# Kernel optimization log

Measured on AMD Instinct MI355X. Metric: run time of the kernel, lower is better.

Reference implementation:

```python
import jax, jax.numpy as jnp
import numpy as np

B, L, D, H = 2, 2048, 1024, 16
HD = D // H


def setup_inputs() -> dict:
    key = jax.random.key(0)
    ks = jax.random.split(key, 12)
    s = 1.0 / np.sqrt(D)
    inp = {
        "q": jax.random.normal(ks[0], (B, L, D), jnp.float32),
        "k": jax.random.normal(ks[1], (B, L, D), jnp.float32),
        "v": jax.random.normal(ks[2], (B, L, D), jnp.float32),
        "mask": jnp.zeros((B, L), dtype=bool),  # True = masked out
        "Wq": jax.random.normal(ks[3], (D, D), jnp.float32) * s,
        "bq": jnp.zeros((D,), jnp.float32),
        "Wk": jax.random.normal(ks[4], (D, D), jnp.float32) * s,
        "bk": jnp.zeros((D,), jnp.float32),
        "Wv": jax.random.normal(ks[5], (D, D), jnp.float32) * s,
        "bv": jnp.zeros((D,), jnp.float32),
        "Wo": jax.random.normal(ks[6], (D, D), jnp.float32) * s,
        "bo": jnp.zeros((D,), jnp.float32),
    }
    return inp


def reference(q, k, v, mask, Wq, bq, Wk, bk, Wv, bv, Wo, bo):
    # linear projections (torch Linear: x @ W.T + b), split into heads: [B,H,L,HD]
    def proj(x, W, b):
        y = jnp.einsum('bld,ed->ble', x, W) + b
        return y.reshape(x.shape[0], x.shape[1], H, HD).transpose(0, 2, 1, 3)

    Q = proj(q, Wq, bq)
    K = proj(k, Wk, bk)
    V = proj(v, Wv, bv)

    scale = 1.0 / np.sqrt(HD).astype(np.float32)
    scores = jnp.einsum('bhqd,bhkd->bhqk', Q, K) * scale  # [B,H,Lq,Lk]
    # mask [B,Lk] -> broadcast over heads and query positions
    scores = jnp.where(mask[:, None, None, :], -jnp.inf, scores)
    attn = jax.nn.softmax(scores, axis=-1)
    out = jnp.einsum('bhqk,bhkd->bhqd', attn, V)  # [B,H,Lq,HD]
    out = out.transpose(0, 2, 1, 3).reshape(q.shape[0], q.shape[1], D)
    return jnp.einsum('bld,ed->ble', out, Wo) + bo
```

## Files before the change

### kernel.cpp

```cpp
#include <hip/hip_runtime.h>

#define LSEQ 2048
#define DMODEL 1024
#define NHEAD 16
#define HDIM 64

typedef __attribute__((ext_vector_type(8))) short bf16x8;
typedef __attribute__((ext_vector_type(4))) float f32x4;
typedef __attribute__((ext_vector_type(16))) float f32x16;
typedef unsigned int u32;
typedef unsigned short u16;
typedef unsigned long long u64;

static __device__ __forceinline__ u16 f2bf(float x) {
    return (u16)((__builtin_bit_cast(u32, x) + 0x8000u) >> 16);
}

static __device__ __forceinline__ u32 f2bf_pk(float hi, float lo) {
    u32 a = __builtin_bit_cast(u32, hi) + 0x8000u;
    u32 b = __builtin_bit_cast(u32, lo) + 0x8000u;
#if __has_builtin(__builtin_amdgcn_perm)
    return __builtin_amdgcn_perm(a, b, 0x07060302u);
#else
    return (a & 0xFFFF0000u) | (b >> 16);
#endif
}

static __device__ __forceinline__ float fast_exp2(float x) {
#if __has_builtin(__builtin_amdgcn_exp2f)
    return __builtin_amdgcn_exp2f(x);
#else
    return __expf(x * 0.6931471805599453f);
#endif
}

static __device__ __forceinline__ void gll16(const void* g, void* l) {
    __builtin_amdgcn_global_load_lds(
        (const __attribute__((address_space(1))) u32*)g,
        (__attribute__((address_space(3))) u32*)l, 16, 0, 0);
}

template <int N>
static __device__ __forceinline__ void vwait() {
    asm volatile("s_waitcnt vmcnt(%0)" :: "n"(N) : "memory");
}

__global__ __launch_bounds__(256) void conv_all(
    const float* __restrict__ q, const float* __restrict__ k, const float* __restrict__ v,
    const float* __restrict__ w0, const float* __restrict__ w1,
    const float* __restrict__ w2, const float* __restrict__ w3,
    u16* __restrict__ Qf, u16* __restrict__ Kf, u16* __restrict__ Vf,
    u16* __restrict__ o0, u16* __restrict__ o1, u16* __restrict__ o2,
    u16* __restrict__ o3) {
    const int bid = blockIdx.x;
    const float* s; u16* d; int off;
    if (bid < 12288) {
        const int z = bid >> 12;
        off = bid & 4095;
        if (z == 0)      { s = q; d = Qf; }
        else if (z == 1) { s = k; d = Kf; }
        else             { s = v; d = Vf; }
    } else {
        const int t = bid - 12288;
        const int z = t >> 10;
        off = t & 1023;
        if (z == 0)      { s = w0; d = o0; }
        else if (z == 1) { s = w1; d = o1; }
        else if (z == 2) { s = w2; d = o2; }
        else             { s = w3; d = o3; }
    }
    const int i = (off * 256 + threadIdx.x) * 4;
    float4 x = *(const float4*)(s + i);
    uint2 r;
    r.x = f2bf_pk(x.y, x.x);
    r.y = f2bf_pk(x.w, x.z);
    *(uint2*)(d + i) = r;
}

template <int OUT_MODE, int BN>
__device__ __forceinline__ void mfma_gemm(u16* __restrict__ sm,
                                          const u16* __restrict__ Xb,
                                          const u16* __restrict__ Wb,
                                          const float* __restrict__ bias,
                                          void* __restrict__ Yv, float scale) {
    constexpr int NB = BN / 32;
    constexpr int LPT = (BN == 128) ? 4 : 3;
    constexpr int ASZ = 4096;
    constexpr int BSZ = BN * 32;
    constexpr int NT = DMODEL / 32;
    u16* As = sm;
    u16* Bs = sm + 3 * ASZ;

    const int tid = threadIdx.x;
    const int wave = tid >> 6, lane = tid & 63;
    const int l16 = lane & 15, quad = lane >> 4;
    const int wm = (wave >> 1) * 64, wn = (wave & 1) * (BN / 2);
    const int m0 = blockIdx.x * 128, n0 = blockIdx.y * BN;

    const u16* Xr = Xb + (size_t)(m0 + (tid >> 2)) * DMODEL + (tid & 3) * 8;
    const u16* Wr = Wb + (size_t)(n0 + (tid >> 2)) * DMODEL + (tid & 3) * 8;
    const int t8 = tid * 8;

    auto stage = [&](int kt, int slot) {
        const int k0 = kt * 32;
        u16* Ab = As + slot * ASZ;
        u16* Bb = Bs + slot * BSZ;
        gll16(Xr + k0, Ab + t8);
        gll16(Xr + (size_t)64 * DMODEL + k0, Ab + 2048 + t8);
        gll16(Wr + k0, Bb + t8);
        if (BN == 128)
            gll16(Wr + (size_t)64 * DMODEL + k0, Bb + 2048 + t8);
    };

    f32x4 acc[4][NB];
    #pragma unroll
    for (int i = 0; i < 4; ++i)
        #pragma unroll
        for (int j = 0; j < NB; ++j)
            #pragma unroll
            for (int r = 0; r < 4; ++r) acc[i][j][r] = 0.0f;

    auto compute = [&](int kt) {
        const u16* Ac = As + (kt % 3) * ASZ;
        const u16* Bc = Bs + (kt % 3) * BSZ;
        bf16x8 af[4], bf[NB];
        #pragma unroll
        for (int mb = 0; mb < 4; ++mb)
            af[mb] = *(const bf16x8*)(Ac + (wm + mb * 16 + l16) * 32 + quad * 8);
        #pragma unroll
        for (int nb = 0; nb < NB; ++nb)
            bf[nb] = *(const bf16x8*)(Bc + (wn + nb * 16 + l16) * 32 + quad * 8);
        #pragma unroll
        for (int mb = 0; mb < 4; ++mb)
            #pragma unroll
            for (int nb = 0; nb < NB; ++nb)
                acc[mb][nb] = __builtin_amdgcn_mfma_f32_16x16x32_bf16(
                    af[mb], bf[nb], acc[mb][nb], 0, 0, 0);
    };

    stage(0, 0);
    stage(1, 1);

    #pragma unroll 1
    for (int kt = 0; kt < NT - 1; ++kt) {
        vwait<LPT>();
        __builtin_amdgcn_s_barrier();
        if (kt + 2 < NT) stage(kt + 2, (kt + 2) % 3);
        compute(kt);
    }
    vwait<0>();
    __builtin_amdgcn_s_barrier();
    compute(NT - 1);

    #pragma unroll
    for (int nb = 0; nb < NB; ++nb) {
        const int n = n0 + wn + nb * 16 + l16;
        const float bn = bias[n];
        #pragma unroll
        for (int mb = 0; mb < 4; ++mb) {
            const int mb0 = m0 + wm + mb * 16 + quad * 4;
            if (OUT_MODE == 2) {
                u16* Y = (u16*)Yv;
                uint2 rr;
                rr.x = f2bf_pk((acc[mb][nb][1] + bn) * scale, (acc[mb][nb][0] + bn) * scale);
                rr.y = f2bf_pk((acc[mb][nb][3] + bn) * scale, (acc[mb][nb][2] + bn) * scale);
                const int bb = mb0 >> 11, l = mb0 & 2047;
                const int h = n >> 6, hd = n & 63;
                *(uint2*)(Y + ((size_t)((bb * NHEAD + h) * HDIM) + hd) * LSEQ + l) = rr;
            } else {
                #pragma unroll
                for (int r = 0; r < 4; ++r) {
                    const int m = mb0 + r;
                    const float val = (acc[mb][nb][r] + bn) * scale;
                    if (OUT_MODE == 0) {
                        u16* Y = (u16*)Yv;
                        const int bb = m >> 11, l = m & 2047;
                        const int h = n >> 6, hd = n & 63;
                        Y[(((size_t)(bb * NHEAD + h) * LSEQ + l) * HDIM) + hd] = f2bf(val);
                    } else {
                        float* Y = (float*)Yv;
                        Y[(size_t)m * DMODEL + n] = val;
                    }
                }
            }
        }
    }
}

#define QSCALE (0.125f * 1.4426950408889634f)

__global__ __launch_bounds__(256) void qkv_gemm(
    const u16* __restrict__ Qf, const u16* __restrict__ Kf, const u16* __restrict__ Vf,
    const u16* __restrict__ Wqb, const u16* __restrict__ Wkb, const u16* __restrict__ Wvb,
    const float* __restrict__ bq, const float* __restrict__ bk, const float* __restrict__ bv,
    u16* __restrict__ Qp, u16* __restrict__ Kp, u16* __restrict__ Vtp) {
    __shared__ alignas(16) u16 sm[24576];
    if (blockIdx.z == 0)      mfma_gemm<0, 128>(sm, Qf, Wqb, bq, (void*)Qp, QSCALE);
    else if (blockIdx.z == 1) mfma_gemm<0, 128>(sm, Kf, Wkb, bk, (void*)Kp, 1.0f);
    else                      mfma_gemm<2, 128>(sm, Vf, Wvb, bv, (void*)Vtp, 1.0f);
}

__global__ __launch_bounds__(256) void out_gemm(
    const u16* __restrict__ AOb, const u16* __restrict__ Wob,
    const float* __restrict__ bo, float* __restrict__ out) {
    __shared__ alignas(16) u16 sm[18432];
    mfma_gemm<1, 64>(sm, AOb, Wob, bo, (void*)out, 1.0f);
}

#define KT 128
#define NTILE (LSEQ / KT)

__global__ __launch_bounds__(512, 2) void attn_mfma(
    const u16* __restrict__ Qp, const u16* __restrict__ Kp,
    const u16* __restrict__ Vtp, const unsigned char* __restrict__ mask,
    u16* __restrict__ AOb) {
    __shared__ alignas(16) u16 smem[40960];

    const int tid = threadIdx.x;
    const int wave = tid >> 6;
    const int lane = tid & 63;
    const int l32 = lane & 31;
    const int half = lane >> 5;
    const int bh = blockIdx.x;
    const int b = bh >> 4;
    const int h = bh & 15;
    const int q0 = blockIdx.y * 256;
    const int qw = q0 + wave * 32;

    const u16* Qg = Qp + ((size_t)bh * LSEQ + qw) * HDIM;
    const u16* Kg = Kp + (size_t)bh * LSEQ * HDIM;
    const u16* Vtg = Vtp + (size_t)bh * HDIM * LSEQ;
    const unsigned char* mg = mask + (size_t)b * LSEQ;

    bf16x8 qf[4];
    #pragma unroll
    for (int dc = 0; dc < 4; ++dc)
        qf[dc] = *(const bf16x8*)(Qg + (size_t)l32 * HDIM + dc * 16 + half * 8);

    f32x16 o0 = {}, o1 = {};
    const f32x16 zc = {};
    float ls[4] = {0.0f, 0.0f, 0.0f, 0.0f};

    auto stageK = [&](int ktile, int slot) {
        const int k0 = ktile * KT;
        u16* Kb = smem + slot * 8192;
        #pragma unroll
        for (int j = 0; j < 2; ++j) {
            const int cid = j * 512 + tid;
            const int key = cid >> 3, pc = cid & 7, c = pc ^ (key & 7);
            gll16(Kg + (size_t)(k0 + key) * HDIM + c * 8, Kb + cid * 8);
        }
    };
    auto stageV = [&](int ktile, int slot) {
        const int k0 = ktile * KT;
        u16* Vb = smem + 16384 + slot * 8192;
        #pragma unroll
        for (int j = 0; j < 2; ++j) {
            const int cid = j * 512 + tid;
            const int d = cid >> 4, pc = cid & 15, c = pc ^ (d & 15);
            gll16(Vtg + (size_t)d * LSEQ + k0 + c * 8, Vb + cid * 8);
        }
    };

    stageK(0, 0); stageV(0, 0);

    const u64* mg8 = (const u64*)mg;
    const u64 mm = mg8[lane] | mg8[lane + 64] | mg8[lane + 128] | mg8[lane + 192];
    const bool mask_any = __any((int)(mm != 0ULL));

    __syncthreads();

    u32 pk[4][8];

    for (int kt = 0; kt < NTILE; ++kt) {
        if (kt + 1 < NTILE) {
            stageK(kt + 1, (kt + 1) & 1);
            stageV(kt + 1, (kt + 1) % 3);
        }
        const u16* Kb = smem + (kt & 1) * 8192;

        f32x16 st[4];
        #pragma unroll
        for (int kb = 0; kb < 4; ++kb) {
            const int key = kb * 32 + l32;
            const int phys = half ^ (key & 7);
            bf16x8 kf = *(const bf16x8*)(Kb + key * 64 + phys * 8);
            st[kb] = __builtin_amdgcn_mfma_f32_32x32x16_bf16(kf, qf[0], zc, 0, 0, 0);
        }
        #pragma unroll
        for (int dc = 1; dc < 4; ++dc)
            #pragma unroll
            for (int kb = 0; kb < 4; ++kb) {
                const int key = kb * 32 + l32;
                const int phys = (dc * 2 + half) ^ (key & 7);
                bf16x8 kf = *(const bf16x8*)(Kb + key * 64 + phys * 8);
                st[kb] = __builtin_amdgcn_mfma_f32_32x32x16_bf16(kf, qf[dc], st[kb], 0, 0, 0);
            }

        if (kt > 0) {
            const u16* Vbp = smem + 16384 + ((kt + 2) % 3) * 8192;
            #pragma unroll
            for (int c = 0; c < 8; ++c) {
                const int kb = c >> 1, wb = 4 * (c & 1);
                bf16x8 pb = __builtin_bit_cast(bf16x8, *(uint4*)&pk[kb][wb]);
                {
                    const int d = l32;
                    const int phys = (c * 2 + half) ^ (d & 15);
                    bf16x8 va = *(const bf16x8*)(Vbp + d * 128 + phys * 8);
                    o0 = __builtin_amdgcn_mfma_f32_32x32x16_bf16(va, pb, o0, 0, 0, 0);
                }
                {
                    const int d = 32 + l32;
                    const int phys = (c * 2 + half) ^ (d & 15);
                    bf16x8 va = *(const bf16x8*)(Vbp + d * 128 + phys * 8);
                    o1 = __builtin_amdgcn_mfma_f32_32x32x16_bf16(va, pb, o1, 0, 0, 0);
                }
            }
        }

        if (mask_any) {
            const int k0 = kt * KT;
            const int mb0 = mg[k0 + lane];
            const int mb1 = mg[k0 + 64 + lane];
            const float b0f = mb0 ? -1e30f : 0.0f;
            const float b1f = mb1 ? -1e30f : 0.0f;
            #pragma unroll
            for (int kb = 0; kb < 4; ++kb)
                #pragma unroll
                for (int r = 0; r < 16; ++r) {
                    const int key = kb * 32 + (r & 3) + 8 * (r >> 2) + 4 * half;
                    const float bv = __shfl((kb < 2) ? b0f : b1f, key & 63, 64);
                    st[kb][r] += bv;
                }
        }

        u32 pkn[4][8];
        #pragma unroll
        for (int kb = 0; kb < 4; ++kb)
            #pragma unroll
            for (int w = 0; w < 8; ++w) {
                const float plo = fast_exp2(st[kb][2 * w]);
                const float phi = fast_exp2(st[kb][2 * w + 1]);
                ls[kb] += plo + phi;
                pkn[kb][w] = f2bf_pk(phi, plo);
            }
        #pragma unroll
        for (int kb = 0; kb < 4; ++kb)
            #pragma unroll
            for (int wb = 0; wb < 8; wb += 4) {
#if __has_builtin(__builtin_amdgcn_permlane32_swap)
                auto r02 = __builtin_amdgcn_permlane32_swap(
                    (int)pkn[kb][wb],     (int)pkn[kb][wb + 2], false, false);
                auto r13 = __builtin_amdgcn_permlane32_swap(
                    (int)pkn[kb][wb + 1], (int)pkn[kb][wb + 3], false, false);
                pk[kb][wb]     = (u32)r02[0]; pk[kb][wb + 2] = (u32)r02[1];
                pk[kb][wb + 1] = (u32)r13[0]; pk[kb][wb + 3] = (u32)r13[1];
#else
                const u32 ta = half ? pkn[kb][wb] : pkn[kb][wb + 2];
                const u32 tb = half ? pkn[kb][wb + 1] : pkn[kb][wb + 3];
                const u32 xa = __shfl_xor((int)ta, 32, 64);
                const u32 xb = __shfl_xor((int)tb, 32, 64);
                pk[kb][wb]     = half ? xa : pkn[kb][wb];
                pk[kb][wb + 1] = half ? xb : pkn[kb][wb + 1];
                pk[kb][wb + 2] = half ? pkn[kb][wb + 2] : xa;
                pk[kb][wb + 3] = half ? pkn[kb][wb + 3] : xb;
#endif
            }

        __syncthreads();
    }

    {
        const u16* Vbp = smem + 16384 + ((NTILE - 1) % 3) * 8192;
        #pragma unroll
        for (int c = 0; c < 8; ++c) {
            const int kb = c >> 1, wb = 4 * (c & 1);
            bf16x8 pb = __builtin_bit_cast(bf16x8, *(uint4*)&pk[kb][wb]);
            {
                const int d = l32;
                const int phys = (c * 2 + half) ^ (d & 15);
                bf16x8 va = *(const bf16x8*)(Vbp + d * 128 + phys * 8);
                o0 = __builtin_amdgcn_mfma_f32_32x32x16_bf16(va, pb, o0, 0, 0, 0);
            }
            {
                const int d = 32 + l32;
                const int phys = (c * 2 + half) ^ (d & 15);
                bf16x8 va = *(const bf16x8*)(Vbp + d * 128 + phys * 8);
                o1 = __builtin_amdgcn_mfma_f32_32x32x16_bf16(va, pb, o1, 0, 0, 0);
            }
        }
    }

    const float l_l = (ls[0] + ls[1]) + (ls[2] + ls[3]);
    const float l_tot = l_l + __shfl_xor(l_l, 32, 64);
    const float inv = 1.0f / l_tot;
    __syncthreads();
    u16* T = smem;
    #pragma unroll
    for (int nb = 0; nb < 2; ++nb)
        #pragma unroll
        for (int rp = 0; rp < 8; ++rp) {
            const int r = rp * 2;
            const int d = nb * 32 + (r & 3) + 8 * (r >> 2) + 4 * half;
            const float vlo = (nb ? o1[r] : o0[r]) * inv;
            const float vhi = (nb ? o1[r + 1] : o0[r + 1]) * inv;
            *(u32*)(T + (wave * 32 + l32) * 72 + d) = f2bf_pk(vhi, vlo);
        }
    __syncthreads();
    #pragma unroll
    for (int i = 0; i < 4; ++i) {
        const int cid = i * 512 + tid;
        const int row = cid >> 3, ch = cid & 7;
        bf16x8 val = *(const bf16x8*)(T + row * 72 + ch * 8);
        *(bf16x8*)(AOb + ((size_t)(b * LSEQ + q0 + row) * DMODEL) + h * HDIM + ch * 8) = val;
    }
}

extern "C" void kernel_launch(void* const* d_in, const int* in_sizes, int n_in,
                              void* d_out, int out_size, void* d_ws, size_t ws_size,
                              hipStream_t stream) {
    (void)in_sizes; (void)n_in; (void)out_size; (void)ws_size;
    const float* q  = (const float*)d_in[0];
    const float* k  = (const float*)d_in[1];
    const float* v  = (const float*)d_in[2];
    const unsigned char* mask = (const unsigned char*)d_in[3];
    const float* Wq = (const float*)d_in[4];
    const float* bq = (const float*)d_in[5];
    const float* Wk = (const float*)d_in[6];
    const float* bk = (const float*)d_in[7];
    const float* Wv = (const float*)d_in[8];
    const float* bv = (const float*)d_in[9];
    const float* Wo = (const float*)d_in[10];
    const float* bo = (const float*)d_in[11];
    float* out = (float*)d_out;

    u16* ws16 = (u16*)d_ws;
    const size_t M4 = (size_t)4 * 1024 * 1024;
    const size_t M1 = (size_t)1024 * 1024;
    u16* Qf  = ws16;
    u16* Kf  = ws16 + M4;
    u16* Vf  = ws16 + 2 * M4;
    u16* Qp  = ws16 + 3 * M4;
    u16* Kp  = ws16 + 4 * M4;
    u16* Vtp = ws16 + 5 * M4;
    u16* AOb = ws16 + 6 * M4;
    u16* Wqb = ws16 + 7 * M4;
    u16* Wkb = ws16 + 7 * M4 + M1;
    u16* Wvb = ws16 + 7 * M4 + 2 * M1;
    u16* Wob = ws16 + 7 * M4 + 3 * M1;

    conv_all<<<dim3(16384), 256, 0, stream>>>(q, k, v, Wq, Wk, Wv, Wo,
                                              Qf, Kf, Vf, Wqb, Wkb, Wvb, Wob);
    qkv_gemm<<<dim3(32, 8, 3), 256, 0, stream>>>(Qf, Kf, Vf, Wqb, Wkb, Wvb,
                                                 bq, bk, bv, Qp, Kp, Vtp);
    attn_mfma<<<dim3(32, 8), 512, 0, stream>>>(Qp, Kp, Vtp, mask, AOb);
    out_gemm<<<dim3(32, 16), 256, 0, stream>>>(AOb, Wob, bo, out);
}
```

Measured before the change: 213.0 us.

## Split attention over two key halves and combine partial outputs in a new kernel

Launches the attention kernel with a second grid dimension that processes half of the key tiles each, writing unnormalized bf16 partial outputs and per-row softmax sums into reused workspace. A new combine kernel adds the two partials and normalizes by the summed denominators before the output projection. This is meant to double the number of attention blocks so the GPU's compute units are better occupied, at the cost of extra memory traffic, an extra launch, and an additional bf16 rounding of partials.

```diff
diff --git a/kernel.cpp b/kernel.cpp
--- a/kernel.cpp
+++ b/kernel.cpp
@@ -24,6 +24,10 @@
 #else
     return (a & 0xFFFF0000u) | (b >> 16);
 #endif
+}
+
+static __device__ __forceinline__ float bf2f(short s) {
+    return __builtin_bit_cast(float, (u32)((u16)s) << 16);
 }
 
 static __device__ __forceinline__ float fast_exp2(float x) {
@@ -209,11 +213,12 @@
 
 #define KT 128
 #define NTILE (LSEQ / KT)
-
-__global__ __launch_bounds__(512, 2) void attn_mfma(
+#define HTILE (NTILE / 2)
+
+__global__ __launch_bounds__(512, 4) void attn_mfma(
     const u16* __restrict__ Qp, const u16* __restrict__ Kp,
     const u16* __restrict__ Vtp, const unsigned char* __restrict__ mask,
-    u16* __restrict__ AOb) {
+    u16* __restrict__ P0, u16* __restrict__ P1, float* __restrict__ lbuf) {
     __shared__ alignas(16) u16 smem[40960];
 
     const int tid = threadIdx.x;
@@ -226,6 +231,11 @@
     const int h = bh & 15;
     const int q0 = blockIdx.y * 256;
     const int qw = q0 + wave * 32;
+    const int z = blockIdx.z;
+    const int kt0 = z * HTILE, kt1 = kt0 + HTILE;
+
+    u16* Pz = z ? P1 : P0;
+    float* lb = lbuf + z * (32 * LSEQ);
 
     const u16* Qg = Qp + ((size_t)bh * LSEQ + qw) * HDIM;
     const u16* Kg = Kp + (size_t)bh * LSEQ * HDIM;
@@ -262,7 +272,7 @@
         }
     };
 
-    stageK(0, 0); stageV(0, 0);
+    stageK(kt0, kt0 & 1); stageV(kt0, kt0 % 3);
 
     const u64* mg8 = (const u64*)mg;
     const u64 mm = mg8[lane] | mg8[lane + 64] | mg8[lane + 128] | mg8[lane + 192];
@@ -272,8 +282,8 @@
 
     u32 pk[4][8];
 
-    for (int kt = 0; kt < NTILE; ++kt) {
-        if (kt + 1 < NTILE) {
+    for (int kt = kt0; kt < kt1; ++kt) {
+        if (kt + 1 < kt1) {
             stageK(kt + 1, (kt + 1) & 1);
             stageV(kt + 1, (kt + 1) % 3);
         }
@@ -297,7 +307,7 @@
                 st[kb] = __builtin_amdgcn_mfma_f32_32x32x16_bf16(kf, qf[dc], st[kb], 0, 0, 0);
             }
 
-        if (kt > 0) {
+        if (kt > kt0) {
             const u16* Vbp = smem + 16384 + ((kt + 2) % 3) * 8192;
             #pragma unroll
             for (int c = 0; c < 8; ++c) {
@@ -371,7 +381,7 @@
     }
 
     {
-        const u16* Vbp = smem + 16384 + ((NTILE - 1) % 3) * 8192;
+        const u16* Vbp = smem + 16384 + ((kt1 - 1) % 3) * 8192;
         #pragma unroll
         for (int c = 0; c < 8; ++c) {
             const int kb = c >> 1, wb = 4 * (c & 1);
@@ -393,7 +403,7 @@
 
     const float l_l = (ls[0] + ls[1]) + (ls[2] + ls[3]);
     const float l_tot = l_l + __shfl_xor(l_l, 32, 64);
-    const float inv = 1.0f / l_tot;
+    if (!half) lb[bh * LSEQ + qw + l32] = l_tot;
     __syncthreads();
     u16* T = smem;
     #pragma unroll
@@ -402,8 +412,8 @@
         for (int rp = 0; rp < 8; ++rp) {
             const int r = rp * 2;
             const int d = nb * 32 + (r & 3) + 8 * (r >> 2) + 4 * half;
-            const float vlo = (nb ? o1[r] : o0[r]) * inv;
-            const float vhi = (nb ? o1[r + 1] : o0[r + 1]) * inv;
+            const float vlo = (nb ? o1[r] : o0[r]);
+            const float vhi = (nb ? o1[r + 1] : o0[r + 1]);
             *(u32*)(T + (wave * 32 + l32) * 72 + d) = f2bf_pk(vhi, vlo);
         }
     __syncthreads();
@@ -412,8 +422,30 @@
         const int cid = i * 512 + tid;
         const int row = cid >> 3, ch = cid & 7;
         bf16x8 val = *(const bf16x8*)(T + row * 72 + ch * 8);
-        *(bf16x8*)(AOb + ((size_t)(b * LSEQ + q0 + row) * DMODEL) + h * HDIM + ch * 8) = val;
-    }
+        *(bf16x8*)(Pz + ((size_t)(b * LSEQ + q0 + row) * DMODEL) + h * HDIM + ch * 8) = val;
+    }
+}
+
+__global__ __launch_bounds__(256) void combine(
+    const u16* __restrict__ P0, const u16* __restrict__ P1,
+    const float* __restrict__ lbuf, u16* __restrict__ AOb) {
+    const int c = (blockIdx.x * 256 + threadIdx.x) * 8;
+    const int bl = c >> 10;
+    const int k = c & 1023;
+    const int h = k >> 6;
+    const int b = bl >> 11, l = bl & 2047;
+    const int li = ((b << 4) + h) * LSEQ + l;
+    const float inv = 1.0f / (lbuf[li] + lbuf[32 * LSEQ + li]);
+    bf16x8 x0 = *(const bf16x8*)(P0 + c);
+    bf16x8 x1 = *(const bf16x8*)(P1 + c);
+    u32 r[4];
+    #pragma unroll
+    for (int j = 0; j < 4; ++j) {
+        const float lo = (bf2f(x0[2 * j]) + bf2f(x1[2 * j])) * inv;
+        const float hi = (bf2f(x0[2 * j + 1]) + bf2f(x1[2 * j + 1])) * inv;
+        r[j] = f2bf_pk(hi, lo);
+    }
+    *(uint4*)(AOb + c) = *(uint4*)r;
 }
 
 extern "C" void kernel_launch(void* const* d_in, const int* in_sizes, int n_in,
@@ -449,10 +481,15 @@
     u16* Wvb = ws16 + 7 * M4 + 2 * M1;
     u16* Wob = ws16 + 7 * M4 + 3 * M1;
 
+    u16* P0 = Qf;
+    u16* P1 = Kf;
+    float* lbuf = (float*)Vf;
+
     conv_all<<<dim3(16384), 256, 0, stream>>>(q, k, v, Wq, Wk, Wv, Wo,
                                               Qf, Kf, Vf, Wqb, Wkb, Wvb, Wob);
     qkv_gemm<<<dim3(32, 8, 3), 256, 0, stream>>>(Qf, Kf, Vf, Wqb, Wkb, Wvb,
                                                  bq, bk, bv, Qp, Kp, Vtp);
-    attn_mfma<<<dim3(32, 8), 512, 0, stream>>>(Qp, Kp, Vtp, mask, AOb);
+    attn_mfma<<<dim3(32, 8, 2), 512, 0, stream>>>(Qp, Kp, Vtp, mask, P0, P1, lbuf);
+    combine<<<dim3(2048), 256, 0, stream>>>(P0, P1, lbuf, AOb);
     out_gemm<<<dim3(32, 16), 256, 0, stream>>>(AOb, Wob, bo, out);
 }
```

Result: slower. 350.7 us (+64.7%).
